# Performance work log

Hardware: AMD Instinct MI355X
Metric: run time of the kernel (lower is better)

## Reference

```python
import jax, jax.numpy as jnp
import numpy as np

B, S, E = 4, 4096, 1024
HEADS, WINDOW = 16, 128
HEAD_DIM = E // HEADS


def setup_inputs() -> dict:
    key = jax.random.key(0)
    ks = jax.random.split(key, 6)
    x = jax.random.normal(ks[0], (B, S, E), dtype=jnp.float32)
    attn_mask = jnp.ones((B, 1, S), dtype=jnp.float32)
    scale = 1.0 / np.sqrt(E)
    Wq = jax.random.normal(ks[1], (E, E), dtype=jnp.float32) * scale
    Wk = jax.random.normal(ks[2], (E, E), dtype=jnp.float32) * scale
    Wv = jax.random.normal(ks[3], (E, E), dtype=jnp.float32) * scale
    Wo = jax.random.normal(ks[4], (E, E), dtype=jnp.float32) * scale
    return {"x": x, "attn_mask": attn_mask, "Wq": Wq, "Wk": Wk, "Wv": Wv, "Wo": Wo}


def _look_around(t, axis_windows=2):
    # t: [..., nw, w, ...]; returns concat of windows [i-1, i, i+1] along the
    # intra-window axis, zero-padded at the boundaries.
    pad = [(0, 0)] * t.ndim
    pad[axis_windows] = (1, 1)
    tp = jnp.pad(t, pad)
    nw = t.shape[axis_windows]
    def sl(start):
        idx = [slice(None)] * t.ndim
        idx[axis_windows] = slice(start, start + nw)
        return tp[tuple(idx)]
    return jnp.concatenate([sl(0), sl(1), sl(2)], axis=axis_windows + 1)


def _local_attention(q, k, v, key_mask, window):
    # q,k,v: [b, h, n, d]; key_mask: [b, n] bool. Non-causal, look_backward=1,
    # look_forward=1 (lucidrains LocalAttention defaults for causal=False).
    b, h, n, d = q.shape
    nw = n // window
    scale = d ** -0.5
    qb = q.reshape(b, h, nw, window, d) * scale
    kb = k.reshape(b, h, nw, window, d)
    vb = v.reshape(b, h, nw, window, d)
    k_look = _look_around(kb, axis_windows=2)  # [b,h,nw,3w,d]
    v_look = _look_around(vb, axis_windows=2)
    # mask: user key mask AND in-bounds (padded boundary windows are invalid)
    mb = key_mask.reshape(b, nw, window)
    m_look = _look_around(mb, axis_windows=1)  # [b,nw,3w]
    m_look = m_look[:, None, :, None, :]       # [b,1,nw,1,3w]
    scores = jnp.einsum('bhnwd,bhnkd->bhnwk', qb, k_look)
    mask_value = -jnp.finfo(scores.dtype).max
    scores = jnp.where(m_look, scores, mask_value)
    attn = jax.nn.softmax(scores, axis=-1)
    out = jnp.einsum('bhnwk,bhnkd->bhnwd', attn, v_look)
    return out.reshape(b, h, n, d)


def reference(x, attn_mask, Wq, Wk, Wv, Wo):
    b, c, e = x.shape
    h, d = HEADS, HEAD_DIM
    q = jnp.einsum('bce,ef->bcf', x, Wq.T).reshape(b, c, h, d).transpose(0, 2, 1, 3)
    k = jnp.einsum('bce,ef->bcf', x, Wk.T).reshape(b, c, h, d).transpose(0, 2, 1, 3)
    v = jnp.einsum('bce,ef->bcf', x, Wv.T).reshape(b, c, h, d).transpose(0, 2, 1, 3)
    key_mask = attn_mask[:, 0, :] > 0  # [b, c] bool
    attended = _local_attention(q, k, v, key_mask, WINDOW)
    attended = attended.transpose(0, 2, 1, 3).reshape(b, c, h * d)
    return jnp.einsum('bcf,fe->bce', attended, Wo.T)
```

## Files before the change

kernel.cpp:

```cpp
#include <hip/hip_runtime.h>
#include <stdint.h>

typedef __bf16 bf16_t;
typedef __bf16 bf16x8 __attribute__((ext_vector_type(8)));
typedef __bf16 bf16x4 __attribute__((ext_vector_type(4)));
typedef float f32x4 __attribute__((ext_vector_type(4)));

__device__ __forceinline__ f32x4 mfma16(bf16x8 a, bf16x8 b, f32x4 c) {
  return __builtin_amdgcn_mfma_f32_16x16x32_bf16(a, b, c, 0, 0, 0);
}

__device__ __forceinline__ void g2l16(const void* g, void* l) {
  __builtin_amdgcn_global_load_lds((const __attribute__((address_space(1))) void*)g,
                                   (__attribute__((address_space(3))) void*)l, 16, 0, 0);
}

#define FENCE() asm volatile("" ::: "memory")

__global__ void __launch_bounds__(256) cvt_f32_bf16(const float* __restrict__ in,
                                                    bf16_t* __restrict__ out) {
  long i = ((long)blockIdx.x * 256 + threadIdx.x) * 8;
  float4 f0 = *(const float4*)(in + i);
  float4 f1 = *(const float4*)(in + i + 4);
  bf16x8 v;
  v[0] = (bf16_t)f0.x; v[1] = (bf16_t)f0.y; v[2] = (bf16_t)f0.z; v[3] = (bf16_t)f0.w;
  v[4] = (bf16_t)f1.x; v[5] = (bf16_t)f1.y; v[6] = (bf16_t)f1.z; v[7] = (bf16_t)f1.w;
  *(bf16x8*)(out + i) = v;
}

template <typename OutT>
__global__ void __launch_bounds__(512, 2) gemm256(const bf16_t* __restrict__ A,
                                                  const bf16_t* __restrict__ Bt,
                                                  OutT* __restrict__ C,
                                                  int M, int N, int K, int NBN) {
  extern __shared__ char smem[];
  const int t = threadIdx.x;
  const int w = t >> 6, l = t & 63;
  const int lr = l & 15, lg = l >> 4;
  const int wm = w >> 2, wn = w & 3;

  const int nwg = gridDim.x;
  const int flat = blockIdx.x;
  const int swz = (flat & 7) * (nwg >> 3) + (flat >> 3);
  const int bm = swz / NBN, bn = swz % NBN;
  const long rowA0 = (long)bm * 256;
  const long colC0 = (long)bn * 256;
  const int KT = K >> 6;

  const int colSwz = ((l & 7) ^ (l >> 3)) * 8;
  const bf16_t* gA = A + (rowA0 + w * 32 + (l >> 3)) * (long)K + colSwz;
  const bf16_t* gB = Bt + (colC0 + w * 32 + (l >> 3)) * (long)K + colSwz;
  const long K8 = (long)K * 8;

  const int sx0 = (lg ^ (lr & 7)) * 16;
  const int sx1 = ((4 + lg) ^ (lr & 7)) * 16;
  const int aRow = (wm * 128 + lr) * 128;
  const int bRow = 32768 + (wn * 64 + lr) * 128;

  f32x4 acc[8][4] = {};

#define STAGE_A(buf, kt)                                          \
  {                                                               \
    char* _d = smem + (buf) * 65536 + w * 4096;                   \
    const long _ko = (long)(kt) * 64;                             \
    g2l16(gA + _ko, _d);                                          \
    g2l16(gA + K8 + _ko, _d + 1024);                              \
    g2l16(gA + 2 * K8 + _ko, _d + 2048);                          \
    g2l16(gA + 3 * K8 + _ko, _d + 3072);                          \
  }
#define STAGE_B(buf, kt)                                          \
  {                                                               \
    char* _d = smem + (buf) * 65536 + 32768 + w * 4096;           \
    const long _ko = (long)(kt) * 64;                             \
    g2l16(gB + _ko, _d);                                          \
    g2l16(gB + K8 + _ko, _d + 1024);                              \
    g2l16(gB + 2 * K8 + _ko, _d + 2048);                          \
    g2l16(gB + 3 * K8 + _ko, _d + 3072);                          \
  }

  STAGE_A(0, 0); STAGE_B(0, 0);
  FENCE();
  asm volatile("s_waitcnt vmcnt(0)" ::: "memory");
  __builtin_amdgcn_s_barrier();

  for (int kt = 0; kt < KT; ++kt) {
    const char* sb = smem + (kt & 1) * 65536;
    const int nb = (kt + 1) & 1;
    const bool ds = (kt + 1) < KT;

    bf16x8 bfr[4][2];

    {
      bf16x8 a0[2][2];
#pragma unroll
      for (int j = 0; j < 4; ++j) {
        bfr[j][0] = *(const bf16x8*)(sb + bRow + j * 2048 + sx0);
        bfr[j][1] = *(const bf16x8*)(sb + bRow + j * 2048 + sx1);
      }
#pragma unroll
      for (int i = 0; i < 2; ++i) {
        a0[i][0] = *(const bf16x8*)(sb + aRow + i * 2048 + sx0);
        a0[i][1] = *(const bf16x8*)(sb + aRow + i * 2048 + sx1);
      }
      if (ds) STAGE_A(nb, kt + 1);
      FENCE();
      __builtin_amdgcn_s_barrier();
      asm volatile("s_waitcnt lgkmcnt(0)" ::: "memory");
      __builtin_amdgcn_sched_barrier(0);
      __builtin_amdgcn_s_setprio(1);
#pragma unroll
      for (int i = 0; i < 2; ++i)
#pragma unroll
        for (int j = 0; j < 4; ++j) {
          acc[i][j] = mfma16(a0[i][0], bfr[j][0], acc[i][j]);
          acc[i][j] = mfma16(a0[i][1], bfr[j][1], acc[i][j]);
        }
      __builtin_amdgcn_s_setprio(0);
      __builtin_amdgcn_sched_barrier(0);
      FENCE();
      __builtin_amdgcn_s_barrier();
    }

#pragma unroll
    for (int p = 1; p < 4; ++p) {
      bf16x8 ap[2][2];
#pragma unroll
      for (int i = 0; i < 2; ++i) {
        ap[i][0] = *(const bf16x8*)(sb + aRow + (2 * p + i) * 2048 + sx0);
        ap[i][1] = *(const bf16x8*)(sb + aRow + (2 * p + i) * 2048 + sx1);
      }
      if (p == 1 && ds) STAGE_B(nb, kt + 1);
      FENCE();
      __builtin_amdgcn_s_barrier();
      asm volatile("s_waitcnt lgkmcnt(0)" ::: "memory");
      __builtin_amdgcn_sched_barrier(0);
      __builtin_amdgcn_s_setprio(1);
#pragma unroll
      for (int i = 0; i < 2; ++i)
#pragma unroll
        for (int j = 0; j < 4; ++j) {
          acc[2 * p + i][j] = mfma16(ap[i][0], bfr[j][0], acc[2 * p + i][j]);
          acc[2 * p + i][j] = mfma16(ap[i][1], bfr[j][1], acc[2 * p + i][j]);
        }
      __builtin_amdgcn_s_setprio(0);
      __builtin_amdgcn_sched_barrier(0);
      FENCE();
      if (p == 3 && ds) {
        asm volatile("s_waitcnt vmcnt(0)" ::: "memory");
      }
      __builtin_amdgcn_s_barrier();
    }
  }

#pragma unroll
  for (int i = 0; i < 8; ++i)
#pragma unroll
    for (int j = 0; j < 4; ++j)
#pragma unroll
      for (int r = 0; r < 4; ++r) {
        long row = rowA0 + wm * 128 + i * 16 + lg * 4 + r;
        long col = colC0 + wn * 64 + j * 16 + lr;
        C[row * (long)N + col] = (OutT)acc[i][j][r];
      }
#undef STAGE_A
#undef STAGE_B
}

__global__ void __launch_bounds__(512, 4) swa3(const bf16_t* __restrict__ QK,
                                               const bf16_t* __restrict__ VT,
                                               const float* __restrict__ amask,
                                               bf16_t* __restrict__ Att) {
  extern __shared__ char lds[];
  bf16_t* Ks = (bf16_t*)lds;
  bf16_t* Vs = (bf16_t*)(lds + 16384);
  float* bias = (float*)(lds + 32768);
  const int t = threadIdx.x, w = t >> 6, l = t & 63, lr = l & 15, lg = l >> 4;
  char* Psw = lds + 33280 + w * 4352;

  const int idx = (blockIdx.x & 7) * 256 + (blockIdx.x >> 3);
  const int n = idx & 31, h = (idx >> 5) & 15, b = idx >> 9;
  const long rowQ = (long)b * 4096 + n * 128;

  bf16x8 qf[2];
#pragma unroll
  for (int ks = 0; ks < 2; ++ks)
    qf[ks] = *(const bf16x8*)&QK[(rowQ + w * 16 + lr) * 2048 + h * 64 + ks * 32 + lg * 8];

  f32x4 oT[4] = {};
  float m_run = -1e30f, l_run = 0.f;

  const int kcLo = (n > 0) ? n - 1 : 0;
  const int kcHi = (n < 31) ? n + 1 : 31;
  const long kbase0 = (long)b * 4096 + (long)kcLo * 128;

  const int kcol = ((t & 7) ^ ((t >> 3) & 7)) * 8;
  const bf16_t* gK0 = QK + (kbase0 + (t >> 3)) * 2048 + 1024 + h * 64 + kcol;
  const bf16_t* gK1 = gK0 + (long)64 * 2048;
  const int vrow = t >> 4;
  const int vcol = ((t & 15) ^ ((t >> 4) & 15)) * 8;
  const bf16_t* gV0 = VT + ((long)h * 64 + vrow) * 16384 + (long)b * 4096 + (long)kcLo * 128 + vcol;
  const bf16_t* gV1 = gV0 + (long)32 * 16384;
  const float* gM = amask + kbase0 + (t & 31) * 4;

  bf16_t* lK0 = Ks + t * 8;
  bf16_t* lK1 = Ks + 4096 + t * 8;
  bf16_t* lV0 = Vs + t * 8;
  bf16_t* lV1 = Vs + 4096 + t * 8;

  const int nch = kcHi - kcLo + 1;
  for (int c = 0; c < nch; ++c) {
    __syncthreads();
    g2l16(gK0, lK0); g2l16(gK1, lK1);
    g2l16(gV0, lV0); g2l16(gV1, lV1);
    if (t < 32) {
      float4 mv = *(const float4*)gM;
      float4 bv;
      bv.x = mv.x > 0.f ? 0.f : -1e30f;
      bv.y = mv.y > 0.f ? 0.f : -1e30f;
      bv.z = mv.z > 0.f ? 0.f : -1e30f;
      bv.w = mv.w > 0.f ? 0.f : -1e30f;
      *(float4*)&bias[t * 4] = bv;
    }
    FENCE();
    asm volatile("s_waitcnt vmcnt(0)" ::: "memory");
    __syncthreads();

    f32x4 s[8];
#pragma unroll
    for (int kb = 0; kb < 8; ++kb) {
      f32x4 z = {};
#pragma unroll
      for (int ks = 0; ks < 2; ++ks) {
        bf16x8 kA = *(const bf16x8*)&Ks[(kb * 16 + lr) * 64 + (((ks * 4 + lg) ^ (lr & 7)) * 8)];
        z = mfma16(kA, qf[ks], z);
      }
      s[kb] = z;
    }

    float mt = -3e30f;
#pragma unroll
    for (int kb = 0; kb < 8; ++kb) {
      f32x4 bb = *(const f32x4*)&bias[kb * 16 + lg * 4];
#pragma unroll
      for (int r = 0; r < 4; ++r) {
        float sv = s[kb][r] * 0.125f + bb[r];
        s[kb][r] = sv;
        mt = fmaxf(mt, sv);
      }
    }
    mt = fmaxf(mt, __shfl_xor(mt, 16));
    mt = fmaxf(mt, __shfl_xor(mt, 32));
    float mnew = fmaxf(m_run, mt);
    float alpha = __expf(m_run - mnew);
    m_run = mnew;
    float rs = 0.f;
#pragma unroll
    for (int kb = 0; kb < 8; ++kb)
#pragma unroll
      for (int r = 0; r < 4; ++r) {
        float p = __expf(s[kb][r] - mnew);
        s[kb][r] = p;
        rs += p;
      }
    rs += __shfl_xor(rs, 16);
    rs += __shfl_xor(rs, 32);
    l_run = l_run * alpha + rs;
#pragma unroll
    for (int df = 0; df < 4; ++df)
#pragma unroll
      for (int r = 0; r < 4; ++r) oT[df][r] *= alpha;

#pragma unroll
    for (int kb = 0; kb < 8; ++kb) {
      bf16x4 pv;
      pv[0] = (bf16_t)s[kb][0]; pv[1] = (bf16_t)s[kb][1];
      pv[2] = (bf16_t)s[kb][2]; pv[3] = (bf16_t)s[kb][3];
      *(bf16x4*)(Psw + lr * 272 + kb * 32 + lg * 8) = pv;
    }
    asm volatile("s_waitcnt lgkmcnt(0)" ::: "memory");
    __builtin_amdgcn_sched_barrier(0);

#pragma unroll
    for (int ks = 0; ks < 4; ++ks) {
      bf16x8 pB = *(const bf16x8*)(Psw + lr * 272 + ks * 64 + lg * 16);
#pragma unroll
      for (int df = 0; df < 4; ++df) {
        bf16x8 vA = *(const bf16x8*)&Vs[(df * 16 + lr) * 128 + (((ks * 4 + lg) ^ lr) * 8)];
        oT[df] = mfma16(vA, pB, oT[df]);
      }
    }

    gK0 += (long)128 * 2048; gK1 += (long)128 * 2048;
    gV0 += 128; gV1 += 128;
    gM += 128;
  }

  float inv = 1.f / l_run;
#pragma unroll
  for (int df = 0; df < 4; ++df) {
    bf16x4 ov;
#pragma unroll
    for (int r = 0; r < 4; ++r) ov[r] = (bf16_t)(oT[df][r] * inv);
    *(bf16x4*)(Psw + lr * 272 + df * 32 + lg * 8) = ov;
  }
  asm volatile("s_waitcnt lgkmcnt(0)" ::: "memory");
  __builtin_amdgcn_sched_barrier(0);
  const char* myP = lds + 33280 + w * 4352;
  bf16x8 r0 = *(const bf16x8*)(myP + (l >> 2) * 272 + (l & 3) * 32);
  bf16x8 r1 = *(const bf16x8*)(myP + (l >> 2) * 272 + (l & 3) * 32 + 16);
  long orow = rowQ + w * 16 + (l >> 2);
  bf16_t* op = Att + orow * 1024 + h * 64 + (l & 3) * 16;
  *(bf16x8*)op = r0;
  *(bf16x8*)(op + 8) = r1;
}

extern "C" void kernel_launch(void* const* d_in, const int* in_sizes, int n_in,
                              void* d_out, int out_size, void* d_ws, size_t ws_size,
                              hipStream_t stream) {
  const float* x  = (const float*)d_in[0];
  const float* am = (const float*)d_in[1];
  const float* Wq = (const float*)d_in[2];
  const float* Wk = (const float*)d_in[3];
  const float* Wv = (const float*)d_in[4];
  const float* Wo = (const float*)d_in[5];
  float* out = (float*)d_out;

  char* ws = (char*)d_ws;
  bf16_t* qk  = (bf16_t*)ws;
  bf16_t* vt  = (bf16_t*)(ws + 67108864);
  bf16_t* xbx = (bf16_t*)(ws + 100663296);
  bf16_t* wqk = (bf16_t*)(ws + 134217728);
  bf16_t* wvb = (bf16_t*)(ws + 138412032);
  bf16_t* wob = (bf16_t*)(ws + 140509184);

  const int kSmemG = 131072;
  hipFuncSetAttribute(reinterpret_cast<const void*>(&gemm256<bf16_t>),
                      hipFuncAttributeMaxDynamicSharedMemorySize, kSmemG);
  hipFuncSetAttribute(reinterpret_cast<const void*>(&gemm256<float>),
                      hipFuncAttributeMaxDynamicSharedMemorySize, kSmemG);
  const int kSmemS = 68096;
  hipFuncSetAttribute(reinterpret_cast<const void*>(&swa3),
                      hipFuncAttributeMaxDynamicSharedMemorySize, kSmemS);

  cvt_f32_bf16<<<8192, 256, 0, stream>>>(x, xbx);
  cvt_f32_bf16<<<512, 256, 0, stream>>>(Wq, wqk);
  cvt_f32_bf16<<<512, 256, 0, stream>>>(Wk, wqk + 1048576);
  cvt_f32_bf16<<<512, 256, 0, stream>>>(Wv, wvb);
  cvt_f32_bf16<<<512, 256, 0, stream>>>(Wo, wob);

  gemm256<bf16_t><<<512, 512, kSmemG, stream>>>(xbx, wqk, qk, 16384, 2048, 1024, 8);

  gemm256<bf16_t><<<256, 512, kSmemG, stream>>>(wvb, xbx, vt, 1024, 16384, 1024, 64);

  swa3<<<2048, 512, kSmemS, stream>>>(qk, vt, am, xbx);

  gemm256<float><<<256, 512, kSmemG, stream>>>(xbx, wob, out, 16384, 1024, 1024, 4);
}
```

Baseline: 229.9 us.

## Prefetch next K/V chunks during compute in SWA kernel and coarsen GEMM phases

The sliding-window attention kernel now loads the mask bias for all chunks up front. It prefetches the next chunk's K tile right after the QK MFMAs and the next V tile right after the PV MFMAs, replacing the old load-then-wait-then-compute loop so global loads overlap softmax and MMA work. The GEMM inner loop drops from four barrier-separated A sub-phases to two larger ones, which cuts barriers and holds more A fragments in registers. The changes add register pressure, slightly more LDS, and depend on finely tuned vmcnt waits.

```diff
diff --git a/kernel.cpp b/kernel.cpp
--- a/kernel.cpp
+++ b/kernel.cpp
@@ -91,14 +91,14 @@
     bf16x8 bfr[4][2];
 
     {
-      bf16x8 a0[2][2];
+      bf16x8 a0[4][2];
 #pragma unroll
       for (int j = 0; j < 4; ++j) {
         bfr[j][0] = *(const bf16x8*)(sb + bRow + j * 2048 + sx0);
         bfr[j][1] = *(const bf16x8*)(sb + bRow + j * 2048 + sx1);
       }
 #pragma unroll
-      for (int i = 0; i < 2; ++i) {
+      for (int i = 0; i < 4; ++i) {
         a0[i][0] = *(const bf16x8*)(sb + aRow + i * 2048 + sx0);
         a0[i][1] = *(const bf16x8*)(sb + aRow + i * 2048 + sx1);
       }
@@ -109,7 +109,7 @@
       __builtin_amdgcn_sched_barrier(0);
       __builtin_amdgcn_s_setprio(1);
 #pragma unroll
-      for (int i = 0; i < 2; ++i)
+      for (int i = 0; i < 4; ++i)
 #pragma unroll
         for (int j = 0; j < 4; ++j) {
           acc[i][j] = mfma16(a0[i][0], bfr[j][0], acc[i][j]);
@@ -121,31 +121,30 @@
       __builtin_amdgcn_s_barrier();
     }
 
-#pragma unroll
-    for (int p = 1; p < 4; ++p) {
-      bf16x8 ap[2][2];
-#pragma unroll
-      for (int i = 0; i < 2; ++i) {
-        ap[i][0] = *(const bf16x8*)(sb + aRow + (2 * p + i) * 2048 + sx0);
-        ap[i][1] = *(const bf16x8*)(sb + aRow + (2 * p + i) * 2048 + sx1);
-      }
-      if (p == 1 && ds) STAGE_B(nb, kt + 1);
+    {
+      bf16x8 a1[4][2];
+#pragma unroll
+      for (int i = 0; i < 4; ++i) {
+        a1[i][0] = *(const bf16x8*)(sb + aRow + (4 + i) * 2048 + sx0);
+        a1[i][1] = *(const bf16x8*)(sb + aRow + (4 + i) * 2048 + sx1);
+      }
+      if (ds) STAGE_B(nb, kt + 1);
       FENCE();
       __builtin_amdgcn_s_barrier();
       asm volatile("s_waitcnt lgkmcnt(0)" ::: "memory");
       __builtin_amdgcn_sched_barrier(0);
       __builtin_amdgcn_s_setprio(1);
 #pragma unroll
-      for (int i = 0; i < 2; ++i)
+      for (int i = 0; i < 4; ++i)
 #pragma unroll
         for (int j = 0; j < 4; ++j) {
-          acc[2 * p + i][j] = mfma16(ap[i][0], bfr[j][0], acc[2 * p + i][j]);
-          acc[2 * p + i][j] = mfma16(ap[i][1], bfr[j][1], acc[2 * p + i][j]);
+          acc[4 + i][j] = mfma16(a1[i][0], bfr[j][0], acc[4 + i][j]);
+          acc[4 + i][j] = mfma16(a1[i][1], bfr[j][1], acc[4 + i][j]);
         }
       __builtin_amdgcn_s_setprio(0);
       __builtin_amdgcn_sched_barrier(0);
       FENCE();
-      if (p == 3 && ds) {
+      if (ds) {
         asm volatile("s_waitcnt vmcnt(0)" ::: "memory");
       }
       __builtin_amdgcn_s_barrier();
@@ -175,7 +174,7 @@
   bf16_t* Vs = (bf16_t*)(lds + 16384);
   float* bias = (float*)(lds + 32768);
   const int t = threadIdx.x, w = t >> 6, l = t & 63, lr = l & 15, lg = l >> 4;
-  char* Psw = lds + 33280 + w * 4352;
+  char* Psw = lds + 34304 + w * 4352;
 
   const int idx = (blockIdx.x & 7) * 256 + (blockIdx.x >> 3);
   const int n = idx & 31, h = (idx >> 5) & 15, b = idx >> 9;
@@ -192,38 +191,48 @@
   const int kcLo = (n > 0) ? n - 1 : 0;
   const int kcHi = (n < 31) ? n + 1 : 31;
   const long kbase0 = (long)b * 4096 + (long)kcLo * 128;
+  const int nch = kcHi - kcLo + 1;
 
   const int kcol = ((t & 7) ^ ((t >> 3) & 7)) * 8;
   const bf16_t* gK0 = QK + (kbase0 + (t >> 3)) * 2048 + 1024 + h * 64 + kcol;
-  const bf16_t* gK1 = gK0 + (long)64 * 2048;
   const int vrow = t >> 4;
   const int vcol = ((t & 15) ^ ((t >> 4) & 15)) * 8;
-  const bf16_t* gV0 = VT + ((long)h * 64 + vrow) * 16384 + (long)b * 4096 + (long)kcLo * 128 + vcol;
-  const bf16_t* gV1 = gV0 + (long)32 * 16384;
-  const float* gM = amask + kbase0 + (t & 31) * 4;
+  const bf16_t* gV0 = VT + ((long)h * 64 + vrow) * 16384 + kbase0 + vcol;
 
   bf16_t* lK0 = Ks + t * 8;
   bf16_t* lK1 = Ks + 4096 + t * 8;
   bf16_t* lV0 = Vs + t * 8;
   bf16_t* lV1 = Vs + 4096 + t * 8;
 
-  const int nch = kcHi - kcLo + 1;
+#define STAGE_K(cc)                                               \
+  {                                                               \
+    const bf16_t* _k = gK0 + (long)(cc) * 128 * 2048;             \
+    g2l16(_k, lK0);                                               \
+    g2l16(_k + (long)64 * 2048, lK1);                             \
+  }
+#define STAGE_V(cc)                                               \
+  {                                                               \
+    const bf16_t* _v = gV0 + (long)(cc) * 128;                    \
+    g2l16(_v, lV0);                                               \
+    g2l16(_v + (long)32 * 16384, lV1);                            \
+  }
+
+  STAGE_K(0); STAGE_V(0);
+  if (t < nch * 32) {
+    float4 mv = *(const float4*)(amask + kbase0 + t * 4);
+    float4 bv;
+    bv.x = mv.x > 0.f ? 0.f : -1e30f;
+    bv.y = mv.y > 0.f ? 0.f : -1e30f;
+    bv.z = mv.z > 0.f ? 0.f : -1e30f;
+    bv.w = mv.w > 0.f ? 0.f : -1e30f;
+    *(float4*)&bias[t * 4] = bv;
+  }
+  FENCE();
+  asm volatile("s_waitcnt vmcnt(0)" ::: "memory");
+  __syncthreads();
+
   for (int c = 0; c < nch; ++c) {
-    __syncthreads();
-    g2l16(gK0, lK0); g2l16(gK1, lK1);
-    g2l16(gV0, lV0); g2l16(gV1, lV1);
-    if (t < 32) {
-      float4 mv = *(const float4*)gM;
-      float4 bv;
-      bv.x = mv.x > 0.f ? 0.f : -1e30f;
-      bv.y = mv.y > 0.f ? 0.f : -1e30f;
-      bv.z = mv.z > 0.f ? 0.f : -1e30f;
-      bv.w = mv.w > 0.f ? 0.f : -1e30f;
-      *(float4*)&bias[t * 4] = bv;
-    }
-    FENCE();
-    asm volatile("s_waitcnt vmcnt(0)" ::: "memory");
-    __syncthreads();
+    const bool more = (c + 1) < nch;
 
     f32x4 s[8];
 #pragma unroll
@@ -236,11 +245,14 @@
       }
       s[kb] = z;
     }
+    FENCE();
+    __builtin_amdgcn_s_barrier();
+    if (more) STAGE_K(c + 1);
 
     float mt = -3e30f;
 #pragma unroll
     for (int kb = 0; kb < 8; ++kb) {
-      f32x4 bb = *(const f32x4*)&bias[kb * 16 + lg * 4];
+      f32x4 bb = *(const f32x4*)&bias[c * 128 + kb * 16 + lg * 4];
 #pragma unroll
       for (int r = 0; r < 4; ++r) {
         float sv = s[kb][r] * 0.125f + bb[r];
@@ -280,6 +292,11 @@
     asm volatile("s_waitcnt lgkmcnt(0)" ::: "memory");
     __builtin_amdgcn_sched_barrier(0);
 
+    FENCE();
+    if (more) asm volatile("s_waitcnt vmcnt(2)" ::: "memory");
+    else      asm volatile("s_waitcnt vmcnt(0)" ::: "memory");
+    __builtin_amdgcn_s_barrier();
+
 #pragma unroll
     for (int ks = 0; ks < 4; ++ks) {
       bf16x8 pB = *(const bf16x8*)(Psw + lr * 272 + ks * 64 + lg * 16);
@@ -289,11 +306,17 @@
         oT[df] = mfma16(vA, pB, oT[df]);
       }
     }
-
-    gK0 += (long)128 * 2048; gK1 += (long)128 * 2048;
-    gV0 += 128; gV1 += 128;
-    gM += 128;
-  }
+    FENCE();
+    __builtin_amdgcn_s_barrier();
+    if (more) {
+      STAGE_V(c + 1);
+      FENCE();
+      asm volatile("s_waitcnt vmcnt(2)" ::: "memory");
+      __builtin_amdgcn_s_barrier();
+    }
+  }
+#undef STAGE_K
+#undef STAGE_V
 
   float inv = 1.f / l_run;
 #pragma unroll
@@ -305,7 +328,7 @@
   }
   asm volatile("s_waitcnt lgkmcnt(0)" ::: "memory");
   __builtin_amdgcn_sched_barrier(0);
-  const char* myP = lds + 33280 + w * 4352;
+  const char* myP = lds + 34304 + w * 4352;
   bf16x8 r0 = *(const bf16x8*)(myP + (l >> 2) * 272 + (l & 3) * 32);
   bf16x8 r1 = *(const bf16x8*)(myP + (l >> 2) * 272 + (l & 3) * 32 + 16);
   long orow = rowQ + w * 16 + (l >> 2);
@@ -338,7 +361,7 @@
                       hipFuncAttributeMaxDynamicSharedMemorySize, kSmemG);
   hipFuncSetAttribute(reinterpret_cast<const void*>(&gemm256<float>),
                       hipFuncAttributeMaxDynamicSharedMemorySize, kSmemG);
-  const int kSmemS = 68096;
+  const int kSmemS = 69120;
   hipFuncSetAttribute(reinterpret_cast<const void*>(&swa3),
                       hipFuncAttributeMaxDynamicSharedMemorySize, kSmemS);
 
```

New measurement: 229.7 us. No clear change (-0.1%).
